# Kernel optimization log

Measured on AMD Instinct MI355X. Metric: run time of the kernel, lower is better.

The kernel has to match this reference:

```python
import jax, jax.numpy as jnp
import numpy as np

B, T, C, H, FF, BOT = 2, 2048, 1024, 16, 4096, 64
D = C // H
EPS = 1e-5

def _ln(x, g, b):
    m = jnp.mean(x, axis=-1, keepdims=True)
    v = jnp.mean(jnp.square(x - m), axis=-1, keepdims=True)
    return (x - m) * jax.lax.rsqrt(v + EPS) * g + b

def setup_inputs() -> dict:
    key = jax.random.key(0)
    ks = jax.random.split(key, 20)
    def lin(k, fan_in, shape):
        return jax.random.normal(k, shape, jnp.float32) * (1.0 / np.sqrt(fan_in))
    inp = {
        "x": jax.random.normal(ks[0], (B, T, C), jnp.float32),
        # causal mask: masked_fill where mask == 0
        "attn_mask": jnp.tril(jnp.ones((T, T), jnp.int32))[None, None, :, :],
        "Wq": lin(ks[1], C, (C, C)), "bq": jnp.zeros((C,), jnp.float32),
        "Wk": lin(ks[2], C, (C, C)), "bk": jnp.zeros((C,), jnp.float32),
        "Wv": lin(ks[3], C, (C, C)), "bv": jnp.zeros((C,), jnp.float32),
        "Wo": lin(ks[4], C, (C, C)), "bo": jnp.zeros((C,), jnp.float32),
        "g1": jnp.ones((C,), jnp.float32), "beta1": jnp.zeros((C,), jnp.float32),
        "g2": jnp.ones((C,), jnp.float32), "beta2": jnp.zeros((C,), jnp.float32),
        "W1": lin(ks[5], C, (C, FF)), "bf1": jnp.zeros((FF,), jnp.float32),
        "W2": lin(ks[6], FF, (FF, C)), "bf2": jnp.zeros((C,), jnp.float32),
        "Wd": lin(ks[7], C, (C, BOT)), "bd": jnp.zeros((BOT,), jnp.float32),
        "Wu": lin(ks[8], BOT, (BOT, C)), "bu": jnp.zeros((C,), jnp.float32),
    }
    return inp

def reference(x, attn_mask, Wq, bq, Wk, bk, Wv, bv, Wo, bo,
              g1, beta1, g2, beta2, W1, bf1, W2, bf2, Wd, bd, Wu, bu):
    # --- attention sublayer ---
    xn = _ln(x, g1, beta1)
    q = (xn @ Wq + bq).reshape(B, T, H, D)
    k = (xn @ Wk + bk).reshape(B, T, H, D)
    v = (xn @ Wv + bv).reshape(B, T, H, D)
    scores = jnp.einsum('bthd,bshd->bhts', q, k) / jnp.sqrt(jnp.float32(D))
    scores = jnp.where(attn_mask == 0, -jnp.inf, scores)
    w = jax.nn.softmax(scores, axis=-1)
    attn = jnp.einsum('bhts,bshd->bthd', w, v).reshape(B, T, C)
    x = x + attn @ Wo + bo
    # --- FFN + adapter sublayer ---
    xn2 = _ln(x, g2, beta2)
    h = jax.nn.relu(xn2 @ W1 + bf1) @ W2 + bf2
    h = h + jax.nn.relu(h @ Wd + bd) @ Wu + bu  # adapter residual
    return x + h
```

## Files before the change

### kernel.cpp

```cpp
#include <hip/hip_runtime.h>
#include <cstdint>
#include <cstddef>

typedef unsigned short u16;
typedef __attribute__((ext_vector_type(4))) short short4v;
typedef __attribute__((ext_vector_type(8))) short short8;
typedef __attribute__((ext_vector_type(4))) float f32x4;

__device__ __forceinline__ float bf2f(u16 h) { return __uint_as_float(((unsigned)h) << 16); }
__device__ __forceinline__ u16 f2bf(float f) {
    unsigned u = __float_as_uint(f);
    unsigned r = (u + 0x7fffu + ((u >> 16) & 1u)) >> 16;
    return (u16)r;
}
__device__ __forceinline__ u16 f2bf_fast(float f) {
    return (u16)((__float_as_uint(f) + 0x8000u) >> 16);
}

__device__ __forceinline__ void gl_lds16(const void* g, void* l) {
    __builtin_amdgcn_global_load_lds((const __attribute__((address_space(1))) void*)g,
                                     (__attribute__((address_space(3))) void*)l, 16, 0, 0);
}

__global__ __launch_bounds__(256) void detect_kernel(const unsigned* __restrict__ x,
                                                     int* __restrict__ flag) {
    __shared__ int cnt[256];
    int c = 0;
    for (int i = threadIdx.x; i < 4096; i += 256) {
        unsigned lo = x[i] & 0xFFFFu;
        unsigned e = (lo >> 7) & 0xFFu;
        c += (e >= 100u && e <= 150u) ? 1 : 0;
    }
    cnt[threadIdx.x] = c;
    __syncthreads();
    for (int s = 128; s > 0; s >>= 1) {
        if (threadIdx.x < s) cnt[threadIdx.x] += cnt[threadIdx.x + s];
        __syncthreads();
    }
    if (threadIdx.x == 0) *flag = (cnt[0] > 2048) ? 1 : 0;
}

struct ParamCvt {
    const void* src[12];
    int off[12];
    int n[12];
};
__global__ __launch_bounds__(256) void param_cvt_kernel(ParamCvt pc, float* __restrict__ dst,
                                                        const int* __restrict__ flag) {
    const int bf = *flag;
    const int s = blockIdx.x;
    const void* sp = pc.src[s];
    float* dp = dst + pc.off[s];
    const int n = pc.n[s];
    for (int i = threadIdx.x; i < n; i += 256)
        dp[i] = bf ? bf2f(((const u16*)sp)[i]) : ((const float*)sp)[i];
}

__global__ __launch_bounds__(256) void cvt_x_kernel(const void* __restrict__ x,
                                                    u16* __restrict__ xb,
                                                    const int* __restrict__ flag) {
    const int bf = *flag;
    const int i0 = (blockIdx.x * 256 + threadIdx.x) * 4;
    u16 o[4];
    if (bf) {
        *(uint2*)o = *(const uint2*)((const u16*)x + i0);
    } else {
        float4 f = *(const float4*)((const float*)x + i0);
        o[0] = f2bf(f.x); o[1] = f2bf(f.y); o[2] = f2bf(f.z); o[3] = f2bf(f.w);
    }
    *(uint2*)&xb[i0] = *(uint2*)o;
}

struct TAll {
    const void* src[8];
    u16* dst[8];
    int R[8], C[8];
    int off[8];
};
__global__ __launch_bounds__(256) void transpose_all_kernel(TAll t,
                                                            const int* __restrict__ flag) {
    const int bf = *flag;
    __shared__ u16 tile[32][33];
    int bid = blockIdx.x;
    int m = 0;
#pragma unroll
    for (int i = 1; i < 8; i++) m = (bid >= t.off[i]) ? i : m;
    int local = bid - t.off[m];
    const int R = t.R[m], C = t.C[m];
    const int tilesx = C >> 5;
    const int bx = local % tilesx, by = local / tilesx;
    const void* src = t.src[m];
    u16* dst = t.dst[m];
    const int tx = threadIdx.x & 31, ty = threadIdx.x >> 5;
#pragma unroll
    for (int i = 0; i < 32; i += 8) {
        size_t idx = (size_t)(by * 32 + ty + i) * C + bx * 32 + tx;
        tile[ty + i][tx] = bf ? ((const u16*)src)[idx] : f2bf(((const float*)src)[idx]);
    }
    __syncthreads();
#pragma unroll
    for (int i = 0; i < 32; i += 8)
        dst[(size_t)(bx * 32 + ty + i) * R + by * 32 + tx] = tile[tx][ty + i];
}

__global__ __launch_bounds__(256) void ln_kernel(const u16* __restrict__ X,
                                                 const float* __restrict__ G,
                                                 const float* __restrict__ Be,
                                                 u16* __restrict__ Y) {
    const int row = blockIdx.x;
    const int tid = threadIdx.x;
    const int lane = tid & 63, wave = tid >> 6;
    const u16* xr = X + (size_t)row * 1024;
    u16 vbuf[4];
    *(uint2*)vbuf = *(const uint2*)&xr[tid * 4];
    float f[4];
    float s = 0.f, sq = 0.f;
#pragma unroll
    for (int j = 0; j < 4; j++) { f[j] = bf2f(vbuf[j]); s += f[j]; sq += f[j] * f[j]; }
#pragma unroll
    for (int m = 1; m < 64; m <<= 1) { s += __shfl_xor(s, m, 64); sq += __shfl_xor(sq, m, 64); }
    __shared__ float rs_[4], rq_[4];
    if (lane == 0) { rs_[wave] = s; rq_[wave] = sq; }
    __syncthreads();
    float S = rs_[0] + rs_[1] + rs_[2] + rs_[3];
    float Q2 = rq_[0] + rq_[1] + rq_[2] + rq_[3];
    float mean = S * (1.f / 1024.f);
    float var = Q2 * (1.f / 1024.f) - mean * mean;
    float rstd = rsqrtf(var + 1e-5f);
    u16 o[4];
#pragma unroll
    for (int j = 0; j < 4; j++) {
        int c2 = tid * 4 + j;
        float y = (f[j] - mean) * rstd * G[c2] + Be[c2];
        o[j] = f2bf(y);
    }
    *(uint2*)&Y[(size_t)row * 1024 + tid * 4] = *(uint2*)o;
}

template <int TAG>
__global__ __launch_bounds__(256) void gemm_bt_kernel(const u16* __restrict__ A,
                                                      const u16* __restrict__ Bt,
                                                      const float* __restrict__ bias,
                                                      const u16* __restrict__ res1,
                                                      const u16* __restrict__ res2,
                                                      void* __restrict__ out,
                                                      void* __restrict__ out_k,
                                                      void* __restrict__ out_v,
                                                      int M, int N, int K, int relu, int mode,
                                                      const int* __restrict__ flag) {
    __shared__ __align__(16) u16 As[2][128 * 32];
    __shared__ __align__(16) u16 Bs[2][128 * 32];
    const int tid = threadIdx.x;
    const int wave = tid >> 6, lane = tid & 63;
    const int m0 = blockIdx.y * 128, n0 = blockIdx.x * 128;
    const int wm = (wave >> 1) * 64, wn = (wave & 1) * 64;

    f32x4 acc[4][4];
#pragma unroll
    for (int i = 0; i < 4; i++)
#pragma unroll
        for (int j = 0; j < 4; j++) acc[i][j] = (f32x4){0.f, 0.f, 0.f, 0.f};

    const int lr4 = lane >> 2;
    const int sc4 = ((lane & 3) ^ ((lane >> 3) & 3));

    const int Ksub = K / (int)gridDim.z;
    const int kbeg = blockIdx.z * Ksub;

    auto stage = [&](int k0, int bufi) {
#pragma unroll
        for (int c = 0; c < 2; c++) {
            int rbase = wave * 32 + c * 16;
            int arow = m0 + rbase + lr4;
            int brow = n0 + rbase + lr4;
            if (brow > N - 1) brow = N - 1;
            gl_lds16(A + (size_t)arow * K + k0 + sc4 * 8, &As[bufi][rbase * 32 + lane * 8]);
            gl_lds16(Bt + (size_t)brow * K + k0 + sc4 * 8, &Bs[bufi][rbase * 32 + lane * 8]);
        }
    };

    stage(kbeg, 0);
    __syncthreads();
    const int nk = Ksub >> 5;
    for (int ik = 0; ik < nk; ik++) {
        const int cur = ik & 1;
        if (ik + 1 < nk) stage(kbeg + ((ik + 1) << 5), cur ^ 1);
        short8 af[4], bf[4];
        const int cc = (lane >> 4) ^ ((lane >> 1) & 3);
#pragma unroll
        for (int i = 0; i < 4; i++)
            af[i] = *(const short8*)&As[cur][(wm + i * 16 + (lane & 15)) * 32 + cc * 8];
#pragma unroll
        for (int j = 0; j < 4; j++)
            bf[j] = *(const short8*)&Bs[cur][(wn + j * 16 + (lane & 15)) * 32 + cc * 8];
#pragma unroll
        for (int i = 0; i < 4; i++)
#pragma unroll
            for (int j = 0; j < 4; j++)
                acc[i][j] = __builtin_amdgcn_mfma_f32_16x16x32_bf16(af[i], bf[j], acc[i][j], 0, 0, 0);
        __syncthreads();
    }

    if (mode == 3) {
        float* po = (float*)out + (size_t)blockIdx.z * M * N;
#pragma unroll
        for (int j = 0; j < 4; j++) {
            int col = n0 + wn + j * 16 + (lane & 15);
            if (col >= N) continue;
#pragma unroll
            for (int i = 0; i < 4; i++)
#pragma unroll
                for (int r = 0; r < 4; r++) {
                    int row = m0 + wm + i * 16 + (lane >> 4) * 4 + r;
                    po[(size_t)row * N + col] = acc[i][j][r];
                }
        }
        return;
    }

    const int f32out = (mode == 1) && (*flag == 0);
#pragma unroll
    for (int j = 0; j < 4; j++) {
        int col = n0 + wn + j * 16 + (lane & 15);
        if (col >= N) continue;
        float bv = bias ? bias[col] : 0.f;
#pragma unroll
        for (int i = 0; i < 4; i++) {
#pragma unroll
            for (int r = 0; r < 4; r++) {
                int row = m0 + wm + i * 16 + (lane >> 4) * 4 + r;
                float v = acc[i][j][r] + bv;
                if (relu) v = fmaxf(v, 0.f);
                size_t idx = (size_t)row * N + col;
                if (res1) v += bf2f(res1[idx]);
                if (res2) v += bf2f(res2[idx]);
                if (f32out) ((float*)out)[idx] = v;
                else ((u16*)out)[idx] = f2bf(v);
            }
        }
    }
}

template <int TAG>
__global__ __launch_bounds__(512, 4) void gemm128_kernel(const u16* __restrict__ A,
                                                         const u16* __restrict__ Bt,
                                                         const float* __restrict__ bias,
                                                         const u16* __restrict__ res1,
                                                         const u16* __restrict__ res2,
                                                         void* __restrict__ out,
                                                         void* __restrict__ out_k,
                                                         void* __restrict__ out_v,
                                                         int M, int N, int K, int relu, int mode,
                                                         int swz,
                                                         const int* __restrict__ flag) {
    (void)flag; (void)M;
    __shared__ __align__(16) u16 As[2][2][128 * 32];
    __shared__ __align__(16) u16 Bs[2][2][128 * 32];
    const int tid = threadIdx.x;
    const int wave = tid >> 6, lane = tid & 63;
    const int l15 = lane & 15, quad = lane >> 4;
    const int wr = wave & 3, wc = wave >> 2;
    int bx = blockIdx.x, by = blockIdx.y;
    if (swz) {
        const int gx = gridDim.x;
        const int nwg = gx * gridDim.y;
        const int bid = by * gx + bx;
        const int sbid = (bid & 7) * (nwg >> 3) + (bid >> 3);
        bx = sbid % gx;
        by = sbid / gx;
    }
    const int m0 = by * 128, n0 = bx * 128;
    const int nt = K >> 6;

    const int rsub = lane >> 2;
    const int logc = (lane & 3) ^ ((rsub >> 1) & 3);

    auto stage_pair = [&](int t, int kh) {
        const int buf = t & 1;
        const int kk = (t << 6) + (kh << 5) + logc * 8;
        const int roff = wave * 16 + rsub;
        gl_lds16(A + (size_t)(m0 + roff) * K + kk, &As[buf][kh][wave * 512 + lane * 8]);
        gl_lds16(Bt + (size_t)(n0 + roff) * K + kk, &Bs[buf][kh][wave * 512 + lane * 8]);
    };

    f32x4 acc[2][4];
#pragma unroll
    for (int i = 0; i < 2; i++)
#pragma unroll
        for (int j = 0; j < 4; j++) acc[i][j] = (f32x4){0.f, 0.f, 0.f, 0.f};

    stage_pair(0, 0);
    stage_pair(0, 1);
    stage_pair(1, 0);
    asm volatile("s_waitcnt vmcnt(4)" ::: "memory");
    __builtin_amdgcn_s_barrier();

    const int rx = (l15 >> 1) & 3;
    for (int t = 0; t < nt; t++) {
        const int b = t & 1;
#pragma unroll
        for (int ph = 0; ph < 2; ph++) {
            const int kh = ph;
            short8 af[2], bfr[4];
#pragma unroll
            for (int i = 0; i < 2; i++)
                af[i] = *(const short8*)&As[b][kh][(wr * 32 + i * 16 + l15) * 32 +
                                                   ((quad ^ rx) << 3)];
#pragma unroll
            for (int j = 0; j < 4; j++)
                bfr[j] = *(const short8*)&Bs[b][kh][(wc * 64 + j * 16 + l15) * 32 +
                                                    ((quad ^ rx) << 3)];
            if (ph == 0) { if (t + 1 < nt) stage_pair(t + 1, 1); }
            else         { if (t + 2 < nt) stage_pair(t + 2, 0); }
            __builtin_amdgcn_s_setprio(1);
#pragma unroll
            for (int i = 0; i < 2; i++)
#pragma unroll
                for (int j = 0; j < 4; j++)
                    acc[i][j] = __builtin_amdgcn_mfma_f32_16x16x32_bf16(
                        af[i], bfr[j], acc[i][j], 0, 0, 0);
            __builtin_amdgcn_s_setprio(0);
            if (ph == 0) {
                if (t + 1 < nt) { asm volatile("s_waitcnt vmcnt(4)" ::: "memory"); }
                else            { asm volatile("s_waitcnt vmcnt(0)" ::: "memory"); }
            } else {
                if (t + 2 < nt)      { asm volatile("s_waitcnt vmcnt(4)" ::: "memory"); }
                else if (t + 1 < nt) { asm volatile("s_waitcnt vmcnt(2)" ::: "memory"); }
            }
            __builtin_amdgcn_s_barrier();
        }
    }

    if (mode == 2) {
        const int region = n0 >> 10;
        if (region < 2) {
            u16* o = (u16*)(region == 0 ? out : out_k);
#pragma unroll
            for (int j = 0; j < 4; j++) {
                const int col = n0 + wc * 64 + j * 16 + l15;
                const float bv = bias[col];
                const int cl = col & 1023;
#pragma unroll
                for (int i = 0; i < 2; i++) {
                    const int row0 = m0 + wr * 32 + i * 16 + quad * 4;
#pragma unroll
                    for (int r = 0; r < 4; r++)
                        o[(size_t)(row0 + r) * 1024 + cl] = f2bf(acc[i][j][r] + bv);
                }
            }
        } else {
            u16* o = (u16*)out_v;
#pragma unroll
            for (int j = 0; j < 4; j++) {
                const int col = n0 + wc * 64 + j * 16 + l15;
                const float bv = bias[col];
                const int cl = col & 1023;
                const int h = cl >> 6, d = cl & 63;
#pragma unroll
                for (int i = 0; i < 2; i++) {
                    const int row_base = m0 + wr * 32 + i * 16 + quad * 4;
                    const int bb = row_base >> 11, tt = row_base & 2047;
                    u16 pk[4];
#pragma unroll
                    for (int r = 0; r < 4; r++) pk[r] = f2bf(acc[i][j][r] + bv);
                    *(uint2*)&o[(((size_t)bb * 16 + h) * 64 + d) * 2048 + tt] = *(uint2*)pk;
                }
            }
        }
        return;
    }
#pragma unroll
    for (int j = 0; j < 4; j++) {
        const int col = n0 + wc * 64 + j * 16 + l15;
        const float bv = bias ? bias[col] : 0.f;
#pragma unroll
        for (int i = 0; i < 2; i++) {
            const int row0 = m0 + wr * 32 + i * 16 + quad * 4;
#pragma unroll
            for (int r = 0; r < 4; r++) {
                float v = acc[i][j][r] + bv;
                if (relu) v = fmaxf(v, 0.f);
                const size_t idx = (size_t)(row0 + r) * N + col;
                if (res1) v += bf2f(res1[idx]);
                if (res2) v += bf2f(res2[idx]);
                ((u16*)out)[idx] = f2bf(v);
            }
        }
    }
}

template <int TAG>
__global__ __launch_bounds__(512, 2) void gemm128d_kernel(const u16* __restrict__ A,
                                                          const u16* __restrict__ Bt,
                                                          const float* __restrict__ bias,
                                                          const u16* __restrict__ res1,
                                                          void* __restrict__ out,
                                                          int N, int K, int relu, int swz) {
    __shared__ __align__(16) u16 As[2][2][128 * 64];
    __shared__ __align__(16) u16 Bs[2][2][128 * 64];
    const int tid = threadIdx.x;
    const int wave = tid >> 6, lane = tid & 63;
    const int l15 = lane & 15, quad = lane >> 4;
    const int wr = wave & 3, wc = wave >> 2;
    int bx = blockIdx.x, by = blockIdx.y;
    if (swz) {
        const int gx = gridDim.x;
        const int nwg = gx * gridDim.y;
        const int bid = by * gx + bx;
        const int sbid = (bid & 7) * (nwg >> 3) + (bid >> 3);
        bx = sbid % gx;
        by = sbid / gx;
    }
    const int m0 = by * 128, n0 = bx * 128;
    const int nt = K >> 7;

    const int srow = lane >> 3;
    const int logc = (lane & 7) ^ ((lane >> 4) & 3);

    auto stage_pair = [&](int t, int kh) {
        const int buf = t & 1;
        const int kk = (t << 7) + (kh << 6) + logc * 8;
        const int r0 = wave * 16 + srow;
        u16* da = &As[buf][kh][wave * 1024 + lane * 8];
        u16* db = &Bs[buf][kh][wave * 1024 + lane * 8];
        gl_lds16(A + (size_t)(m0 + r0) * K + kk, da);
        gl_lds16(A + (size_t)(m0 + r0 + 8) * K + kk, da + 512);
        gl_lds16(Bt + (size_t)(n0 + r0) * K + kk, db);
        gl_lds16(Bt + (size_t)(n0 + r0 + 8) * K + kk, db + 512);
    };

    f32x4 acc[2][4];
#pragma unroll
    for (int i = 0; i < 2; i++)
#pragma unroll
        for (int j = 0; j < 4; j++) acc[i][j] = (f32x4){0.f, 0.f, 0.f, 0.f};

    stage_pair(0, 0);
    stage_pair(0, 1);
    stage_pair(1, 0);
    asm volatile("s_waitcnt vmcnt(8)" ::: "memory");
    __builtin_amdgcn_s_barrier();

    const int rx = (l15 >> 1) & 3;
    for (int t = 0; t < nt; t++) {
        const int b = t & 1;
#pragma unroll
        for (int ph = 0; ph < 2; ph++) {
            const int kh = ph;
            short8 af[2][2], bfr[4][2];
#pragma unroll
            for (int ks = 0; ks < 2; ks++) {
                const int ck = ((ks << 2) | (quad ^ rx)) << 3;
#pragma unroll
                for (int i = 0; i < 2; i++)
                    af[i][ks] = *(const short8*)&As[b][kh][(wr * 32 + i * 16 + l15) * 64 + ck];
#pragma unroll
                for (int j = 0; j < 4; j++)
                    bfr[j][ks] = *(const short8*)&Bs[b][kh][(wc * 64 + j * 16 + l15) * 64 + ck];
            }
            if (ph == 0) { if (t + 1 < nt) stage_pair(t + 1, 1); }
            else         { if (t + 2 < nt) stage_pair(t + 2, 0); }
            __builtin_amdgcn_s_setprio(1);
#pragma unroll
            for (int ks = 0; ks < 2; ks++)
#pragma unroll
                for (int i = 0; i < 2; i++)
#pragma unroll
                    for (int j = 0; j < 4; j++)
                        acc[i][j] = __builtin_amdgcn_mfma_f32_16x16x32_bf16(
                            af[i][ks], bfr[j][ks], acc[i][j], 0, 0, 0);
            __builtin_amdgcn_s_setprio(0);
            if (ph == 0) {
                if (t + 1 < nt) { asm volatile("s_waitcnt vmcnt(8)" ::: "memory"); }
                else            { asm volatile("s_waitcnt vmcnt(0)" ::: "memory"); }
            } else {
                if (t + 2 < nt)      { asm volatile("s_waitcnt vmcnt(8)" ::: "memory"); }
                else if (t + 1 < nt) { asm volatile("s_waitcnt vmcnt(4)" ::: "memory"); }
            }
            __builtin_amdgcn_s_barrier();
        }
    }

#pragma unroll
    for (int j = 0; j < 4; j++) {
        const int col = n0 + wc * 64 + j * 16 + l15;
        const float bv = bias ? bias[col] : 0.f;
#pragma unroll
        for (int i = 0; i < 2; i++) {
            const int row0 = m0 + wr * 32 + i * 16 + quad * 4;
#pragma unroll
            for (int r = 0; r < 4; r++) {
                float v = acc[i][j][r] + bv;
                if (relu) v = fmaxf(v, 0.f);
                const size_t idx = (size_t)(row0 + r) * N + col;
                if (res1) v += bf2f(res1[idx]);
                ((u16*)out)[idx] = f2bf(v);
            }
        }
    }
}

template <int TAG>
__global__ __launch_bounds__(256) void reduce_kernel(const float* __restrict__ part,
                                                     int nsplit, size_t MN,
                                                     const float* __restrict__ bias, int N,
                                                     const u16* __restrict__ res1,
                                                     const u16* __restrict__ res2,
                                                     void* __restrict__ out,
                                                     int relu, int final_store,
                                                     const int* __restrict__ flag) {
    const size_t i0 = ((size_t)blockIdx.x * 256 + threadIdx.x) * 4;
    float4 s = *(const float4*)&part[i0];
    for (int z = 1; z < nsplit; z++) {
        float4 p = *(const float4*)&part[(size_t)z * MN + i0];
        s.x += p.x; s.y += p.y; s.z += p.z; s.w += p.w;
    }
    const int col = (int)(i0 & (size_t)(N - 1));
    float v[4] = {s.x, s.y, s.z, s.w};
#pragma unroll
    for (int j = 0; j < 4; j++) {
        v[j] += bias[col + j];
        if (relu) v[j] = fmaxf(v[j], 0.f);
    }
    if (res1) {
        u16 r[4]; *(uint2*)r = *(const uint2*)&res1[i0];
#pragma unroll
        for (int j = 0; j < 4; j++) v[j] += bf2f(r[j]);
    }
    if (res2) {
        u16 r[4]; *(uint2*)r = *(const uint2*)&res2[i0];
#pragma unroll
        for (int j = 0; j < 4; j++) v[j] += bf2f(r[j]);
    }
    if (final_store && (*flag == 0)) {
        *(float4*)&((float*)out)[i0] = (float4){v[0], v[1], v[2], v[3]};
    } else {
        u16 o[4];
#pragma unroll
        for (int j = 0; j < 4; j++) o[j] = f2bf(v[j]);
        *(uint2*)&((u16*)out)[i0] = *(uint2*)o;
    }
}

template <int SPLIT>
__global__ __launch_bounds__(256) void flash_kernel(const u16* __restrict__ Q,
                                                    const u16* __restrict__ Kg,
                                                    const u16* __restrict__ VtG,
                                                    u16* __restrict__ O,
                                                    float* __restrict__ pO,
                                                    float* __restrict__ pL) {
    const int tid = threadIdx.x;
    const int wave = tid >> 6, lane = tid & 63;
    int qb, ch;
    if (SPLIT) {
        const int i = blockIdx.x;
        if (i < 32)      { qb = 31 - (i >> 2); ch = i & 3; }
        else if (i < 56) { const int j = i - 32; qb = 23 - j / 3; ch = j % 3; }
        else if (i < 72) { const int j = i - 56; qb = 15 - (j >> 1); ch = j & 1; }
        else             { qb = 7 - (i - 72); ch = 0; }
    } else {
        qb = 31 - blockIdx.x; ch = 0;
    }
    const int bh = blockIdx.y;
    const int t0 = qb * 64;
    const int steps = qb + 1;
    const int ktbeg = SPLIT ? ch * 8 : 0;
    const int ktend = SPLIT ? (steps < ktbeg + 8 ? steps : ktbeg + 8) : steps;
    const size_t base = ((size_t)(bh >> 4) * 2048) * 1024 + (size_t)(bh & 15) * 64;
    const size_t basev = (size_t)bh * 64 * 2048;

    __shared__ __align__(16) u16 Ks[2][64 * 64];
    __shared__ __align__(16) u16 Vt[2][64 * 64];
#if !__has_builtin(__builtin_amdgcn_mfma_f32_16x16x16bf16_1k)
    __shared__ __align__(16) u16 Ps[4][16 * 72];
#endif

    const int l15 = lane & 15, quad = lane >> 4;
    const int rmin = t0 + wave * 16;

    short8 qf[2];
    {
        const u16* qp = Q + base + (size_t)(rmin + l15) * 1024 + quad * 8;
        qf[0] = *(const short8*)qp;
        qf[1] = *(const short8*)(qp + 32);
    }

    const int slr = lane >> 3;
    const int sc8 = (lane & 7) ^ slr;
    const int rb = wave * 16;

    auto stage = [&](int kt, int bufi) {
        gl_lds16(Kg + base + (size_t)(kt * 64 + rb + slr) * 1024 + sc8 * 8,
                 &Ks[bufi][rb * 64 + lane * 8]);
        gl_lds16(Kg + base + (size_t)(kt * 64 + rb + 8 + slr) * 1024 + sc8 * 8,
                 &Ks[bufi][(rb + 8) * 64 + lane * 8]);
        gl_lds16(VtG + basev + (size_t)(rb + slr) * 2048 + kt * 64 + sc8 * 8,
                 &Vt[bufi][rb * 64 + lane * 8]);
        gl_lds16(VtG + basev + (size_t)(rb + 8 + slr) * 2048 + kt * 64 + sc8 * 8,
                 &Vt[bufi][(rb + 8) * 64 + lane * 8]);
    };

    float l_part = 0.f;
    f32x4 oacc[4];
#pragma unroll
    for (int jt = 0; jt < 4; jt++) oacc[jt] = (f32x4){0.f, 0.f, 0.f, 0.f};

    const float Cs = 0.125f * 1.44269504f;

    stage(ktbeg, 0);
    __syncthreads();

    for (int kt = ktbeg; kt < ktend; kt++) {
        const int cur = kt & 1;
        if (kt + 1 < ktend) stage(kt + 1, cur ^ 1);

        short8 kf[2][4];
#pragma unroll
        for (int st = 0; st < 2; st++)
#pragma unroll
            for (int j = 0; j < 4; j++)
                kf[st][j] = *(const short8*)&Ks[cur][(j * 16 + l15) * 64 +
                                                     (((st * 4 + quad) ^ (l15 & 7)) * 8)];
#if __has_builtin(__builtin_amdgcn_mfma_f32_16x16x16bf16_1k)
        short4v vf[4][4];
#pragma unroll
        for (int j = 0; j < 4; j++) {
            int k8 = j * 2 + (quad >> 1);
#pragma unroll
            for (int jt = 0; jt < 4; jt++) {
                int d = jt * 16 + l15;
                vf[j][jt] = *(const short4v*)&Vt[cur][d * 64 + ((k8 ^ (d & 7)) * 8) +
                                                      (quad & 1) * 4];
            }
        }
#else
        short8 vf[2][4];
#pragma unroll
        for (int st = 0; st < 2; st++)
#pragma unroll
            for (int jt = 0; jt < 4; jt++) {
                int d = jt * 16 + l15;
                vf[st][jt] = *(const short8*)&Vt[cur][d * 64 + (((st * 4 + quad) ^ (d & 7)) * 8)];
            }
#endif

        f32x4 s[4];
#pragma unroll
        for (int j = 0; j < 4; j++) s[j] = (f32x4){0.f, 0.f, 0.f, 0.f};
#pragma unroll
        for (int st = 0; st < 2; st++)
#pragma unroll
            for (int j = 0; j < 4; j++)
                s[j] = __builtin_amdgcn_mfma_f32_16x16x32_bf16(kf[st][j], qf[st], s[j], 0, 0, 0);

        const int qrow = rmin + l15;
        const bool needmask = (kt * 64 + 63 > rmin);
        float lp = l_part;
        short4v pj[4];
#pragma unroll
        for (int j = 0; j < 4; j++) {
            union { short4v v; u16 u[4]; } pk;
#pragma unroll
            for (int r = 0; r < 4; r++) {
                float p = __builtin_amdgcn_exp2f(s[j][r] * Cs);
                int key = kt * 64 + j * 16 + quad * 4 + r;
                if (needmask && key > qrow) p = 0.f;
                lp += p;
                pk.u[r] = f2bf_fast(p);
            }
            pj[j] = pk.v;
        }
        l_part = lp;

#if __has_builtin(__builtin_amdgcn_mfma_f32_16x16x16bf16_1k)
#pragma unroll
        for (int jt = 0; jt < 4; jt++)
#pragma unroll
            for (int j = 0; j < 4; j++)
                oacc[jt] = __builtin_amdgcn_mfma_f32_16x16x16bf16_1k(pj[j], vf[j][jt],
                                                                     oacc[jt], 0, 0, 0);
#else
        u16* Pw = Ps[wave];
#pragma unroll
        for (int j = 0; j < 4; j++)
            *(short4v*)&Pw[l15 * 72 + j * 16 + quad * 4] = pj[j];
#pragma unroll
        for (int st = 0; st < 2; st++) {
            short8 pf = *(const short8*)&Pw[l15 * 72 + st * 32 + quad * 8];
#pragma unroll
            for (int jt = 0; jt < 4; jt++)
                oacc[jt] = __builtin_amdgcn_mfma_f32_16x16x32_bf16(pf, vf[st][jt],
                                                                  oacc[jt], 0, 0, 0);
        }
#endif
        __syncthreads();
    }

    float lf = l_part;
    lf += __shfl_xor(lf, 16, 64);
    lf += __shfl_xor(lf, 32, 64);

    if (SPLIT && steps > 8) {
        const size_t ib = ((size_t)bh * 24 + (qb - 8)) * 4 + ch;
        float* po = pO + ib * 4096;
#pragma unroll
        for (int jt = 0; jt < 4; jt++)
#pragma unroll
            for (int r = 0; r < 4; r++)
                po[(wave * 16 + quad * 4 + r) * 64 + jt * 16 + l15] = oacc[jt][r];
        if (quad == 0) pL[ib * 64 + wave * 16 + l15] = lf;
        return;
    }

    {
        float inv[4];
#pragma unroll
        for (int r = 0; r < 4; r++) inv[r] = 1.f / __shfl(lf, quad * 4 + r, 64);
#pragma unroll
        for (int jt = 0; jt < 4; jt++) {
            int d = jt * 16 + l15;
#pragma unroll
            for (int r = 0; r < 4; r++) {
                int t = rmin + quad * 4 + r;
                O[base + (size_t)t * 1024 + d] = f2bf(oacc[jt][r] * inv[r]);
            }
        }
    }
}

__global__ __launch_bounds__(256) void flash_combine_kernel(const float* __restrict__ pO,
                                                            const float* __restrict__ pL,
                                                            u16* __restrict__ O) {
    const int qj = blockIdx.x;
    const int bh = blockIdx.y;
    const int qb = qj + 8;
    const int nch = (qb >> 3) + 1;
    const int tid = threadIdx.x;
    const int row = tid >> 2;
    const int d0 = (tid & 3) * 16;
    const size_t ib = ((size_t)bh * 24 + qj) * 4;

    float acc[16];
#pragma unroll
    for (int k = 0; k < 16; k++) acc[k] = 0.f;
    float lsum = 0.f;
    for (int c = 0; c < nch; c++) {
        const float* po = pO + (ib + c) * 4096 + row * 64 + d0;
#pragma unroll
        for (int v = 0; v < 4; v++) {
            float4 f = *(const float4*)&po[v * 4];
            acc[v * 4 + 0] += f.x; acc[v * 4 + 1] += f.y;
            acc[v * 4 + 2] += f.z; acc[v * 4 + 3] += f.w;
        }
        lsum += pL[(ib + c) * 64 + row];
    }
    const float inv = 1.f / lsum;
    u16 o[16];
#pragma unroll
    for (int k = 0; k < 16; k++) o[k] = f2bf(acc[k] * inv);
    const size_t base = ((size_t)(bh >> 4) * 2048) * 1024 + (size_t)(bh & 15) * 64;
    const int t = qb * 64 + row;
    u16* op = &O[base + (size_t)t * 1024 + d0];
    *(uint4*)op = ((uint4*)o)[0];
    *(uint4*)(op + 8) = ((uint4*)o)[1];
}

extern "C" void kernel_launch(void* const* d_in, const int* in_sizes, int n_in,
                              void* d_out, int out_size, void* d_ws, size_t ws_size,
                              hipStream_t stream) {
    (void)in_sizes; (void)n_in; (void)out_size;
    const void* x   = d_in[0];
    const void* Wq  = d_in[2];  const void* bq  = d_in[3];
    const void* Wk  = d_in[4];  const void* bk  = d_in[5];
    const void* Wv  = d_in[6];  const void* bv  = d_in[7];
    const void* Wo  = d_in[8];  const void* bo  = d_in[9];
    const void* g1  = d_in[10]; const void* be1 = d_in[11];
    const void* g2  = d_in[12]; const void* be2 = d_in[13];
    const void* W1  = d_in[14]; const void* bf1 = d_in[15];
    const void* W2  = d_in[16]; const void* bf2 = d_in[17];
    const void* Wd  = d_in[18]; const void* bd  = d_in[19];
    const void* Wu  = d_in[20]; const void* bu  = d_in[21];

    uint8_t* w8 = (uint8_t*)d_ws;
    int* flag = (int*)w8;
    float* pf = (float*)(w8 + 64);
    u16* wsb = (u16*)(w8 + 64 + 65536);

    const size_t M1 = 1024ull * 1024ull;
    u16* WqT = wsb;
    u16* WkT = wsb + 1 * M1;
    u16* WvT = wsb + 2 * M1;
    u16* WoT = wsb + 3 * M1;
    u16* W1T = wsb + 4 * M1;
    u16* W2T = wsb + 8 * M1;
    u16* WdT = wsb + 12 * M1;
    u16* WuT = wsb + 12 * M1 + 65536;
    u16* S0  = wsb + 12 * M1 + 131072;
    u16* Areg = S0;
    u16* Breg = S0 + 4 * M1;
    u16* ff1  = S0;
    u16* Creg = S0 + 16 * M1;
    u16* Dreg = S0 + 20 * M1;
    u16* Ereg = S0 + 24 * M1;
    u16* xb = Areg;
    u16* xn = Breg; u16* attn = Breg;
    u16* q = Creg;  u16* xn2 = Creg;  u16* bot = Creg;
    u16* kk_ = Dreg; u16* x1 = Dreg;
    u16* VtG = Ereg; u16* hh = Ereg;

    const size_t arena_bytes = (size_t)(64 + 65536) + (40 * M1 + 131072) * 2;
    float* partf = (float*)(w8 + ((arena_bytes + 255) & ~(size_t)255));
    const size_t need = ((arena_bytes + 255) & ~(size_t)255) + 4ull * 4 * M1 * 4;
    const bool sk = ws_size >= need;
    float* flL = partf + 14 * M1;

    float* bqkv_f = pf + 0;
    float* bo_f  = pf + 3072;
    float* bf1_f = pf + 4096;  float* bf2_f = pf + 8192;
    float* bd_f  = pf + 9216;  float* bu_f  = pf + 9280;
    float* g1_f  = pf + 10304; float* be1_f = pf + 11328;
    float* g2_f  = pf + 12352; float* be2_f = pf + 13376;

    detect_kernel<<<1, 256, 0, stream>>>((const unsigned*)x, flag);

    ParamCvt pc;
    const void* srcs[12] = {bq, bk, bv, bo, bf1, bf2, bd, bu, g1, be1, g2, be2};
    int offs[12] = {0, 1024, 2048, 3072, 4096, 8192, 9216, 9280, 10304, 11328, 12352, 13376};
    int ns[12]   = {1024, 1024, 1024, 1024, 4096, 1024, 64, 1024, 1024, 1024, 1024, 1024};
    for (int i = 0; i < 12; i++) { pc.src[i] = srcs[i]; pc.off[i] = offs[i]; pc.n[i] = ns[i]; }
    param_cvt_kernel<<<12, 256, 0, stream>>>(pc, pf, flag);

    cvt_x_kernel<<<4096, 256, 0, stream>>>(x, xb, flag);

    TAll ta;
    const void* tsrc[8] = {Wq, Wk, Wv, Wo, W1, W2, Wd, Wu};
    u16* tdst[8] = {WqT, WkT, WvT, WoT, W1T, W2T, WdT, WuT};
    int tR[8] = {1024, 1024, 1024, 1024, 1024, 4096, 1024, 64};
    int tC[8] = {1024, 1024, 1024, 1024, 4096, 1024, 64, 1024};
    int acc_off = 0;
    for (int i = 0; i < 8; i++) {
        ta.src[i] = tsrc[i]; ta.dst[i] = tdst[i];
        ta.R[i] = tR[i]; ta.C[i] = tC[i];
        ta.off[i] = acc_off;
        acc_off += (tR[i] >> 5) * (tC[i] >> 5);
    }
    transpose_all_kernel<<<acc_off, 256, 0, stream>>>(ta, flag);

    ln_kernel<<<4096, 256, 0, stream>>>(xb, g1_f, be1_f, xn);
    gemm128_kernel<0><<<dim3(24, 32), 512, 0, stream>>>(xn, WqT, bqkv_f, nullptr, nullptr,
                                                        q, kk_, VtG, 4096, 3072, 1024, 0, 2, 0, flag);
    if (sk) {
        flash_kernel<1><<<dim3(80, 32), 256, 0, stream>>>(q, kk_, VtG, attn, partf, flL);
        flash_combine_kernel<<<dim3(24, 32), 256, 0, stream>>>(partf, flL, attn);
    } else {
        flash_kernel<0><<<dim3(32, 32), 256, 0, stream>>>(q, kk_, VtG, attn, nullptr, nullptr);
    }
    gemm128d_kernel<1><<<dim3(8, 32), 512, 0, stream>>>(attn, WoT, bo_f, xb,
                                                        x1, 1024, 1024, 0, 1);
    ln_kernel<<<4096, 256, 0, stream>>>(x1, g2_f, be2_f, xn2);
    gemm128_kernel<2><<<dim3(32, 32), 512, 0, stream>>>(xn2, W1T, bf1_f, nullptr, nullptr,
                                                        ff1, nullptr, nullptr, 4096, 4096, 1024, 1, 0, 0, flag);
    gemm128d_kernel<3><<<dim3(8, 32), 512, 0, stream>>>(ff1, W2T, bf2_f, nullptr,
                                                        hh, 1024, 4096, 0, 1);
    if (sk) {
        gemm_bt_kernel<4><<<dim3(1, 32, 8), 256, 0, stream>>>(hh, WdT, nullptr, nullptr, nullptr,
                                                              partf, nullptr, nullptr, 4096, 64, 1024, 1, 3, flag);
        reduce_kernel<4><<<256, 256, 0, stream>>>(partf, 8, 256 * 1024, bd_f, 64, nullptr, nullptr,
                                                  bot, 1, 0, flag);
    } else {
        gemm_bt_kernel<4><<<dim3(1, 32), 256, 0, stream>>>(hh, WdT, bd_f, nullptr, nullptr,
                                                           bot, nullptr, nullptr, 4096, 64, 1024, 1, 0, flag);
    }
    gemm_bt_kernel<5><<<dim3(8, 32), 256, 0, stream>>>(bot, WuT, bu_f, hh, x1,
                                                       d_out, nullptr, nullptr, 4096, 1024, 64, 0, 1, flag);
}
```

Baseline: 445.1 us.

## Add 256x128-tile GEMM kernel for FFN up-projection

Adds a new GEMM kernel with a 256x128 output tile per 512-thread block, double-buffered LDS staging through global_load_lds, and XOR-swizzled LDS reads. It replaces the 128x128 GEMM for the W1 projection with ReLU. The larger M tile is meant to raise arithmetic intensity and cut global/L2 traffic for B, at the cost of more accumulator registers and only 512 blocks instead of 1024. The generic kernel's flag-driven path is dropped for this call.

After: 444.8 us. About the same (-0.1%).

```diff
diff --git a/kernel.cpp b/kernel.cpp
--- a/kernel.cpp
+++ b/kernel.cpp
@@ -390,6 +390,100 @@
 }
 
 template <int TAG>
+__global__ __launch_bounds__(512, 2) void gemm256m_kernel(const u16* __restrict__ A,
+                                                          const u16* __restrict__ Bt,
+                                                          const float* __restrict__ bias,
+                                                          void* __restrict__ out,
+                                                          int N, int K, int relu) {
+    __shared__ __align__(16) u16 As[2][2][256 * 32];
+    __shared__ __align__(16) u16 Bs[2][2][128 * 32];
+    const int tid = threadIdx.x;
+    const int wave = tid >> 6, lane = tid & 63;
+    const int l15 = lane & 15, quad = lane >> 4;
+    const int wr = wave >> 1, wc = wave & 1;
+    const int m0 = blockIdx.y * 256, n0 = blockIdx.x * 128;
+    const int nt = K >> 6;
+
+    const int rsub = lane >> 2;
+    const int logc = (lane & 3) ^ ((rsub >> 1) & 3);
+
+    auto stage_pair = [&](int t, int kh) {
+        const int buf = t & 1;
+        const int kk = (t << 6) + (kh << 5) + logc * 8;
+        const int ra = m0 + wave * 32 + rsub;
+        const int rb = n0 + wave * 16 + rsub;
+        u16* da = &As[buf][kh][wave * 1024 + lane * 8];
+        gl_lds16(A + (size_t)ra * K + kk, da);
+        gl_lds16(A + (size_t)(ra + 16) * K + kk, da + 512);
+        gl_lds16(Bt + (size_t)rb * K + kk, &Bs[buf][kh][wave * 512 + lane * 8]);
+    };
+
+    f32x4 acc[4][4];
+#pragma unroll
+    for (int i = 0; i < 4; i++)
+#pragma unroll
+        for (int j = 0; j < 4; j++) acc[i][j] = (f32x4){0.f, 0.f, 0.f, 0.f};
+
+    stage_pair(0, 0);
+    stage_pair(0, 1);
+    stage_pair(1, 0);
+    asm volatile("s_waitcnt vmcnt(6)" ::: "memory");
+    __builtin_amdgcn_s_barrier();
+
+    const int rx = (l15 >> 1) & 3;
+    for (int t = 0; t < nt; t++) {
+        const int b = t & 1;
+#pragma unroll
+        for (int ph = 0; ph < 2; ph++) {
+            const int kh = ph;
+            short8 af[4], bfr[4];
+#pragma unroll
+            for (int i = 0; i < 4; i++)
+                af[i] = *(const short8*)&As[b][kh][(wr * 64 + i * 16 + l15) * 32 +
+                                                   ((quad ^ rx) << 3)];
+#pragma unroll
+            for (int j = 0; j < 4; j++)
+                bfr[j] = *(const short8*)&Bs[b][kh][(wc * 64 + j * 16 + l15) * 32 +
+                                                    ((quad ^ rx) << 3)];
+            if (ph == 0) { if (t + 1 < nt) stage_pair(t + 1, 1); }
+            else         { if (t + 2 < nt) stage_pair(t + 2, 0); }
+            __builtin_amdgcn_s_setprio(1);
+#pragma unroll
+            for (int i = 0; i < 4; i++)
+#pragma unroll
+                for (int j = 0; j < 4; j++)
+                    acc[i][j] = __builtin_amdgcn_mfma_f32_16x16x32_bf16(
+                        af[i], bfr[j], acc[i][j], 0, 0, 0);
+            __builtin_amdgcn_s_setprio(0);
+            if (ph == 0) {
+                if (t + 1 < nt) { asm volatile("s_waitcnt vmcnt(6)" ::: "memory"); }
+                else            { asm volatile("s_waitcnt vmcnt(0)" ::: "memory"); }
+            } else {
+                if (t + 2 < nt)      { asm volatile("s_waitcnt vmcnt(6)" ::: "memory"); }
+                else if (t + 1 < nt) { asm volatile("s_waitcnt vmcnt(3)" ::: "memory"); }
+            }
+            __builtin_amdgcn_s_barrier();
+        }
+    }
+
+#pragma unroll
+    for (int j = 0; j < 4; j++) {
+        const int col = n0 + wc * 64 + j * 16 + l15;
+        const float bv = bias ? bias[col] : 0.f;
+#pragma unroll
+        for (int i = 0; i < 4; i++) {
+            const int row0 = m0 + wr * 64 + i * 16 + quad * 4;
+#pragma unroll
+            for (int r = 0; r < 4; r++) {
+                float v = acc[i][j][r] + bv;
+                if (relu) v = fmaxf(v, 0.f);
+                ((u16*)out)[(size_t)(row0 + r) * N + col] = f2bf(v);
+            }
+        }
+    }
+}
+
+template <int TAG>
 __global__ __launch_bounds__(512, 2) void gemm128d_kernel(const u16* __restrict__ A,
                                                           const u16* __restrict__ Bt,
                                                           const float* __restrict__ bias,
@@ -858,8 +952,8 @@
     gemm128d_kernel<1><<<dim3(8, 32), 512, 0, stream>>>(attn, WoT, bo_f, xb,
                                                         x1, 1024, 1024, 0, 1);
     ln_kernel<<<4096, 256, 0, stream>>>(x1, g2_f, be2_f, xn2);
-    gemm128_kernel<2><<<dim3(32, 32), 512, 0, stream>>>(xn2, W1T, bf1_f, nullptr, nullptr,
-                                                        ff1, nullptr, nullptr, 4096, 4096, 1024, 1, 0, 0, flag);
+    gemm256m_kernel<2><<<dim3(32, 16), 512, 0, stream>>>(xn2, W1T, bf1_f,
+                                                         ff1, 4096, 1024, 1);
     gemm128d_kernel<3><<<dim3(8, 32), 512, 0, stream>>>(ff1, W2T, bf2_f, nullptr,
                                                         hh, 1024, 4096, 0, 1);
     if (sk) {
```
